# Performance work log

Hardware: AMD Instinct MI355X
Metric: run time of the kernel (lower is better)

The kernel has to match this reference:

```python
import jax, jax.numpy as jnp
import numpy as np

B, S, IN_DIM, H, NH, DH, OUT_DIM, K, N_KB, L, DFF = 32, 128, 1024, 1024, 8, 128, 256, 10, 500000, 2, 2048


def setup_inputs() -> dict:
    key = jax.random.key(0)
    ks = jax.random.split(key, 16)
    def rn(k, shape, scale=0.02):
        return jax.random.normal(k, shape, jnp.float32) * scale
    return {
        "x": jax.random.normal(ks[0], (B, S, IN_DIM), jnp.float32),
        "ctx": jax.random.normal(ks[1], (B, 1, IN_DIM), jnp.float32),
        "indices": jax.random.randint(ks[2], (B, S, K), 0, N_KB),
        "KB_embs": jax.random.normal(ks[3], (N_KB, OUT_DIM), jnp.float32),
        "W_in": rn(ks[4], (IN_DIM, H)), "b_in": jnp.zeros((H,), jnp.float32),
        "Wqkv": rn(ks[5], (L, H, 3 * H)), "bqkv": jnp.zeros((L, 3 * H), jnp.float32),
        "Wo": rn(ks[6], (L, H, H)), "bo": jnp.zeros((L, H), jnp.float32),
        "ln1_g": jnp.ones((L, H), jnp.float32), "ln1_b": jnp.zeros((L, H), jnp.float32),
        "W1": rn(ks[7], (L, H, DFF)), "b1": jnp.zeros((L, DFF), jnp.float32),
        "W2": rn(ks[8], (L, DFF, H)), "b2": jnp.zeros((L, H), jnp.float32),
        "ln2_g": jnp.ones((L, H), jnp.float32), "ln2_b": jnp.zeros((L, H), jnp.float32),
        "W_out": rn(ks[9], (H, OUT_DIM)), "b_out": jnp.zeros((OUT_DIM,), jnp.float32),
        "ds_W1": rn(ks[10], (OUT_DIM, OUT_DIM)), "ds_b1": jnp.zeros((OUT_DIM,), jnp.float32),
        "ds_W2": rn(ks[11], (OUT_DIM, 1)), "ds_b2": jnp.zeros((1,), jnp.float32),
        "cs_W1": rn(ks[12], (OUT_DIM, OUT_DIM)), "cs_b1": jnp.zeros((OUT_DIM,), jnp.float32),
        "cs_W2": rn(ks[13], (OUT_DIM, 1)), "cs_b2": jnp.zeros((1,), jnp.float32),
    }


def _ln(x, g, b, eps=1e-5):
    m = x.mean(-1, keepdims=True)
    v = ((x - m) ** 2).mean(-1, keepdims=True)
    return (x - m) * jax.lax.rsqrt(v + eps) * g + b


def _encoder_layer(h, Wqkv, bqkv, Wo, bo, g1, bn1, W1, b1, W2, b2, g2, bn2):
    # h: (Sq, Bt, H). PyTorch default batch_first=False -> axis 0 is the attended
    # sequence axis (here the data batch axis B, exactly as the original code runs).
    Sq, Bt, Hd = h.shape
    q, k, v = jnp.split(h @ Wqkv + bqkv, 3, axis=-1)
    q = q.reshape(Sq, Bt, NH, DH)
    k = k.reshape(Sq, Bt, NH, DH)
    v = v.reshape(Sq, Bt, NH, DH)
    att = jnp.einsum('sbhd,tbhd->bhst', q, k) * (1.0 / (DH ** 0.5))
    att = jax.nn.softmax(att, axis=-1)
    o = jnp.einsum('bhst,tbhd->sbhd', att, v).reshape(Sq, Bt, Hd)
    h = _ln(h + o @ Wo + bo, g1, bn1)          # post-norm, eps=1e-5
    ff = jax.nn.relu(h @ W1 + b1) @ W2 + b2    # default dim_feedforward=2048, relu
    return _ln(h + ff, g2, bn2)


def _forward(x, ctx, indices, KB_embs, W_in, b_in, Wqkv, bqkv, Wo, bo, ln1_g, ln1_b,
             W1, b1, W2, b2, ln2_g, ln2_b, W_out, b_out,
             ds_W1, ds_b1, ds_W2, ds_b2, cs_W1, cs_b1, cs_W2, cs_b2):
    h = jnp.concatenate([ctx, x], axis=1)          # (B, S+1, in_dim)
    h = jax.nn.relu(h @ W_in + b_in)               # mapper head (dropout off in eval)
    for l in range(Wqkv.shape[0]):
        h = _encoder_layer(h, Wqkv[l], bqkv[l], Wo[l], bo[l], ln1_g[l], ln1_b[l],
                           W1[l], b1[l], W2[l], b2[l], ln2_g[l], ln2_b[l])
    out = h @ W_out + b_out                        # (B, S+1, out_dim)
    ctx_e, pred = out[:, :1], out[:, 1:]
    idx = jnp.where(indices < 0, 0, indices)       # indices[indices == -1] = 0
    cand = KB_embs[idx]                            # (B, S, K, out_dim) gather
    d = cand - pred[:, :, None, :]
    c = ctx_e[:, :, None, :] * cand
    ds = jax.nn.relu(d @ ds_W1 + ds_b1) @ ds_W2 + ds_b2   # distance_score (B,S,K,1)
    cs = jax.nn.relu(c @ cs_W1 + cs_b1) @ cs_W2 + cs_b2   # context_score: computed but unused by original output
    del cs
    cand_out = jnp.concatenate([ds, cand], axis=-1)       # (B, S, K, 1+out_dim)
    return pred, cand_out


def reference(x, ctx, indices, KB_embs, W_in, b_in, Wqkv, bqkv, Wo, bo, ln1_g, ln1_b,
              W1, b1, W2, b2, ln2_g, ln2_b, W_out, b_out,
              ds_W1, ds_b1, ds_W2, ds_b2, cs_W1, cs_b1, cs_W2, cs_b2):
    return _forward(x, ctx, indices, KB_embs, W_in, b_in, Wqkv, bqkv, Wo, bo,
                    ln1_g, ln1_b, W1, b1, W2, b2, ln2_g, ln2_b, W_out, b_out,
                    ds_W1, ds_b1, ds_W2, ds_b2, cs_W1, cs_b1, cs_W2, cs_b2)
```

## Files before the change

### kernel.cpp

```cpp
#include <hip/hip_runtime.h>
#include <hip/hip_bf16.h>

typedef __attribute__((ext_vector_type(4))) float f32x4;
typedef __attribute__((ext_vector_type(8))) short s16x8;
typedef __attribute__((ext_vector_type(4))) unsigned short u16x4;
typedef __attribute__((ext_vector_type(8))) __bf16 bf16x8;

#define B_      32
#define S_      128
#define SEQ     129
#define IN_DIM  1024
#define HD      1024
#define NHEAD   8
#define DH      128
#define OUT_DIM 256
#define KC      10
#define DFF     2048
#define MROWS   (B_*SEQ)
#define MPAD    4224
#define NCAND   (B_*S_*KC)

__device__ __forceinline__ short f2bf(float f) {
  unsigned u = __builtin_bit_cast(unsigned, f);
  u += 0x7FFFu + ((u >> 16) & 1u);
  return (short)(u >> 16);
}
__device__ __forceinline__ float bf2f(short s) {
  return __builtin_bit_cast(float, ((unsigned)(unsigned short)s) << 16);
}
__device__ __forceinline__ void gload16(const short* g, short* l) {
  __builtin_amdgcn_global_load_lds(
      (const __attribute__((address_space(1))) unsigned*)g,
      (__attribute__((address_space(3))) unsigned*)l, 16, 0, 0);
}
__device__ __forceinline__ f32x4 mfma16(s16x8 a, s16x8 b, f32x4 c) {
  return __builtin_amdgcn_mfma_f32_16x16x32_bf16(
      __builtin_bit_cast(bf16x8, a), __builtin_bit_cast(bf16x8, b), c, 0, 0, 0);
}

__global__ __launch_bounds__(256) void prologue(
    const float* __restrict__ W_in,  const float* __restrict__ Wqkv,
    const float* __restrict__ Wo,    const float* __restrict__ W1,
    const float* __restrict__ W2,    const float* __restrict__ W_out,
    const float* __restrict__ dsW1,
    short* __restrict__ WinT,  short* __restrict__ WqkvT,
    short* __restrict__ WoT,   short* __restrict__ W1T,
    short* __restrict__ W2T,   short* __restrict__ WoutT,
    short* __restrict__ dsW1T,
    const float* __restrict__ x, const float* __restrict__ ctx,
    short* __restrict__ hin) {
  const int b = blockIdx.x;
  if (b >= 17728) {
    const int r = b - 17728;
    const int bb = r / SEQ, t = r % SEQ;
    const float* src = (t == 0) ? (ctx + (size_t)bb * IN_DIM)
                                : (x + ((size_t)bb * S_ + (t - 1)) * IN_DIM);
    f32x4 v = *(const f32x4*)(src + threadIdx.x * 4);
    u16x4 o;
    o.x = (unsigned short)f2bf(v.x); o.y = (unsigned short)f2bf(v.y);
    o.z = (unsigned short)f2bf(v.z); o.w = (unsigned short)f2bf(v.w);
    *(u16x4*)(hin + (size_t)r * IN_DIM + threadIdx.x * 4) = o;
    return;
  }
  const float* src; short* dst; int K, N, local;
  if (b < 1024)       { src = W_in;  dst = WinT;  K = 1024; N = 1024; local = b; }
  else if (b < 7168)  { int l = (b - 1024) / 3072; local = (b - 1024) % 3072;
                        src = Wqkv + (size_t)l * 1024 * 3072;
                        dst = WqkvT + (size_t)l * 3072 * 1024; K = 1024; N = 3072; }
  else if (b < 9216)  { int l = (b - 7168) / 1024; local = (b - 7168) % 1024;
                        src = Wo + (size_t)l * 1024 * 1024;
                        dst = WoT + (size_t)l * 1024 * 1024; K = 1024; N = 1024; }
  else if (b < 13312) { int l = (b - 9216) / 2048; local = (b - 9216) % 2048;
                        src = W1 + (size_t)l * 1024 * 2048;
                        dst = W1T + (size_t)l * 2048 * 1024; K = 1024; N = 2048; }
  else if (b < 17408) { int l = (b - 13312) / 2048; local = (b - 13312) % 2048;
                        src = W2 + (size_t)l * 2048 * 1024;
                        dst = W2T + (size_t)l * 1024 * 2048; K = 2048; N = 1024; }
  else if (b < 17664) { local = b - 17408; src = W_out; dst = WoutT; K = 1024; N = 256; }
  else                { local = b - 17664; src = dsW1;  dst = dsW1T; K = 256;  N = 256; }
  const int tilesX = N >> 5;
  const int n0 = (local % tilesX) << 5, k0 = (local / tilesX) << 5;

  __shared__ float tile[32][33];
  const int tx = threadIdx.x & 31, ty = threadIdx.x >> 5;
#pragma unroll
  for (int i = 0; i < 4; ++i)
    tile[ty + i * 8][tx] = src[(size_t)(k0 + ty + i * 8) * N + n0 + tx];
  __syncthreads();
#pragma unroll
  for (int i = 0; i < 4; ++i)
    dst[(size_t)(n0 + ty + i * 8) * K + k0 + tx] = f2bf(tile[tx][ty + i * 8]);
}

template <int EPI, bool SPLIT, typename OutT>
__global__ __launch_bounds__(256) void gemm_bt(const short* __restrict__ A,
                                               const short* __restrict__ Bt,
                                               const float* __restrict__ bias,
                                               OutT* __restrict__ C,
                                               short* __restrict__ Pb,
                                               int M, int N, int K,
                                               int gm, int gn, int groupM,
                                               int kper) {
  __shared__ alignas(16) short As0[4096], As1[4096];
  __shared__ alignas(16) short Bs0[4096], Bs1[4096];
  const int tid = threadIdx.x;
  const int lane = tid & 63, wave = tid >> 6;
  const int wr = wave >> 1, wc = wave & 1;

  const int nwg = gm * gn;
  int orig = blockIdx.x;
  int split = 0;
  if constexpr (SPLIT) { split = orig / nwg; orig %= nwg; }
  const int xcd = orig & 7, kk = orig >> 3;
  const int q = nwg >> 3, r = nwg & 7;
  const int wg = (xcd < r ? xcd * (q + 1) : r * (q + 1) + (xcd - r) * q) + kk;
  const int tpg = groupM * gn;
  const int grp = wg / tpg, rem = wg % tpg;
  const int g0 = grp * groupM;
  const int gsz = (groupM < gm - g0) ? groupM : (gm - g0);
  const int bm = (g0 + rem % gsz) * 128;
  const int bn = (rem / gsz) * 128;
  const int kbase = SPLIT ? split * kper : 0;

  const short* pa[2];
  const short* pb[2];
#pragma unroll
  for (int i = 0; i < 2; ++i) {
    const int idx = i * 256 + tid;
    const int rr = idx >> 2, ss = idx & 3, gg = ss ^ ((rr >> 1) & 3);
    pa[i] = A + (size_t)(bm + rr) * K + kbase + gg * 8;
    pb[i] = Bt + (size_t)(bn + rr) * K + kbase + gg * 8;
  }

  auto stage = [&](short* aBuf, short* bBuf, int t) {
    const int kofs = t << 5;
    gload16(pa[0] + kofs, aBuf + wave * 512);
    gload16(pa[1] + kofs, aBuf + 2048 + wave * 512);
    gload16(pb[0] + kofs, bBuf + wave * 512);
    gload16(pb[1] + kofs, bBuf + 2048 + wave * 512);
  };

  const int lrow = lane & 15, ks = lane >> 4;
  const int sx = (lrow >> 1) & 3;
  const int koff = ((ks ^ sx) << 3);

  f32x4 acc[4][4] = {};

  auto compute = [&](const short* as, const short* bs) {
    s16x8 af[4], bfr[4];
#pragma unroll
    for (int m = 0; m < 4; ++m)
      af[m] = *(const s16x8*)&as[(wr * 64 + m * 16 + lrow) * 32 + koff];
#pragma unroll
    for (int n = 0; n < 4; ++n)
      bfr[n] = *(const s16x8*)&bs[(wc * 64 + n * 16 + lrow) * 32 + koff];
#pragma unroll
    for (int m = 0; m < 4; ++m)
#pragma unroll
      for (int n = 0; n < 4; ++n)
        asm("v_mfma_f32_16x16x32_bf16 %0, %1, %2, %0"
            : "+v"(acc[m][n]) : "v"(af[m]), "v"(bfr[n]));
  };

  const int NT = (SPLIT ? kper : K) >> 5;
  stage(As0, Bs0, 0);
  __syncthreads();
  for (int t = 0; t < NT; t += 2) {
    stage(As1, Bs1, t + 1);
    compute(As0, Bs0);
    __syncthreads();
    if (t + 2 < NT) stage(As0, Bs0, t + 2);
    compute(As1, Bs1);
    __syncthreads();
  }

  const int lg4 = ks << 2;
#pragma unroll
  for (int n = 0; n < 4; ++n) {
    const int col = bn + wc * 64 + n * 16 + lrow;
    const float bvx = SPLIT ? 0.f : bias[col];
#pragma unroll
    for (int m = 0; m < 4; ++m) {
#pragma unroll
      for (int r2 = 0; r2 < 4; ++r2) {
        const int row = bm + wr * 64 + m * 16 + lg4 + r2;
        if constexpr (SPLIT) {
          Pb[((size_t)split * MPAD + row) * N + col] = f2bf(acc[m][n][r2]);
        } else {
          if (row < M) {
            float v = acc[m][n][r2] + bvx;
            if (EPI == 1) v = fmaxf(v, 0.f);
            if constexpr (__is_same(OutT, float)) {
              C[(size_t)row * N + col] = v;
            } else {
              C[(size_t)row * N + col] = f2bf(v);
            }
          }
        }
      }
    }
  }
}

template <int EPI>
__global__ __launch_bounds__(256) void reduce_cast(const short* __restrict__ P,
                                                   const float* __restrict__ bias,
                                                   short* __restrict__ out,
                                                   int N, int nsplit) {
  const int row = blockIdx.x;
  for (int c = threadIdx.x * 4; c < N; c += 1024) {
    f32x4 s = *(const f32x4*)(bias + c);
    for (int sp = 0; sp < nsplit; ++sp) {
      u16x4 pv = *(const u16x4*)(P + ((size_t)sp * MPAD + row) * N + c);
      s.x += bf2f((short)pv.x); s.y += bf2f((short)pv.y);
      s.z += bf2f((short)pv.z); s.w += bf2f((short)pv.w);
    }
    if (EPI == 1) {
      s.x = fmaxf(s.x, 0.f); s.y = fmaxf(s.y, 0.f);
      s.z = fmaxf(s.z, 0.f); s.w = fmaxf(s.w, 0.f);
    }
    u16x4 y;
    y.x = (unsigned short)f2bf(s.x); y.y = (unsigned short)f2bf(s.y);
    y.z = (unsigned short)f2bf(s.z); y.w = (unsigned short)f2bf(s.w);
    *(u16x4*)(out + (size_t)row * N + c) = y;
  }
}

__global__ __launch_bounds__(256) void reduce_ln(const short* __restrict__ P,
                                                 const float* __restrict__ bias,
                                                 const float* __restrict__ g,
                                                 const float* __restrict__ bb,
                                                 short* __restrict__ h) {
  const int r = blockIdx.x, tid = threadIdx.x;
  f32x4 s = *(const f32x4*)(bias + tid * 4);
  {
    u16x4 p0 = *(const u16x4*)(P + (size_t)r * 1024 + tid * 4);
    u16x4 p1 = *(const u16x4*)(P + ((size_t)MPAD + r) * 1024 + tid * 4);
    s.x += bf2f((short)p0.x) + bf2f((short)p1.x);
    s.y += bf2f((short)p0.y) + bf2f((short)p1.y);
    s.z += bf2f((short)p0.z) + bf2f((short)p1.z);
    s.w += bf2f((short)p0.w) + bf2f((short)p1.w);
  }
  const u16x4 hv = *(const u16x4*)(h + (size_t)r * 1024 + tid * 4);
  float s0 = s.x + bf2f((short)hv.x);
  float s1 = s.y + bf2f((short)hv.y);
  float s2 = s.z + bf2f((short)hv.z);
  float s3 = s.w + bf2f((short)hv.w);
  float ls = s0 + s1 + s2 + s3;
  float l2 = s0 * s0 + s1 * s1 + s2 * s2 + s3 * s3;
#pragma unroll
  for (int off = 32; off > 0; off >>= 1) {
    ls += __shfl_down(ls, off);
    l2 += __shfl_down(l2, off);
  }
  __shared__ float red[8];
  const int wave = tid >> 6, lane = tid & 63;
  if (lane == 0) { red[wave * 2] = ls; red[wave * 2 + 1] = l2; }
  __syncthreads();
  if (tid == 0) {
    float a = 0.f, b2 = 0.f;
    for (int w = 0; w < 4; ++w) { a += red[w * 2]; b2 += red[w * 2 + 1]; }
    red[0] = a; red[1] = b2;
  }
  __syncthreads();
  const float mean = red[0] * (1.f / HD);
  const float var  = red[1] * (1.f / HD) - mean * mean;
  const float inv  = rsqrtf(var + 1e-5f);
  const f32x4 gv = *(const f32x4*)(g + tid * 4);
  const f32x4 bv = *(const f32x4*)(bb + tid * 4);
  u16x4 y;
  y.x = (unsigned short)f2bf((s0 - mean) * inv * gv.x + bv.x);
  y.y = (unsigned short)f2bf((s1 - mean) * inv * gv.y + bv.y);
  y.z = (unsigned short)f2bf((s2 - mean) * inv * gv.z + bv.z);
  y.w = (unsigned short)f2bf((s3 - mean) * inv * gv.w + bv.w);
  *(u16x4*)(h + (size_t)r * 1024 + tid * 4) = y;
}

__global__ __launch_bounds__(64) void reduce_wout(const short* __restrict__ P,
                                                  const float* __restrict__ bias,
                                                  float* __restrict__ pred) {
  const int r = blockIdx.x;
  const int b = r / SEQ, t = r % SEQ;
  if (t == 0) return;
  const int c = threadIdx.x * 4;
  f32x4 s = *(const f32x4*)(bias + c);
#pragma unroll
  for (int sp = 0; sp < 4; ++sp) {
    u16x4 pv = *(const u16x4*)(P + ((size_t)sp * MPAD + r) * 256 + c);
    s.x += bf2f((short)pv.x); s.y += bf2f((short)pv.y);
    s.z += bf2f((short)pv.z); s.w += bf2f((short)pv.w);
  }
  *(f32x4*)(pred + ((size_t)b * S_ + (t - 1)) * 256 + c) = s;
}

__global__ __launch_bounds__(256) void attention_mfma(const short* __restrict__ qkv,
                                                      short* __restrict__ o) {
  __shared__ alignas(16) short qs[4][32][136];
  __shared__ alignas(16) short ksb[4][32][136];
  __shared__ alignas(16) short vsb[4][32][136];
  __shared__ float psb[4][32][33];
  const int tid = threadIdx.x, lane = tid & 63, w = tid >> 6;
  const int gw = blockIdx.x * 4 + w;
  const int t = gw >> 3, hd = gw & 7;
  short (*q)[136] = qs[w];
  short (*k)[136] = ksb[w];
  short (*v)[136] = vsb[w];
  float (*ps)[33] = psb[w];

#pragma unroll
  for (int c = lane; c < 512; c += 64) {
    const int bb = c >> 4, d8 = (c & 15) << 3;
    const size_t base = ((size_t)(bb * SEQ + t)) * (3 * HD) + hd * DH + d8;
    *(s16x8*)&q[bb][d8] = *(const s16x8*)(qkv + base);
    *(s16x8*)&k[bb][d8] = *(const s16x8*)(qkv + base + HD);
    *(s16x8*)&v[bb][d8] = *(const s16x8*)(qkv + base + 2 * HD);
  }

  const int lrow = lane & 15, ksl = lane >> 4;
  const float scale = 0.08838834764831845f;

  f32x4 pacc[2][2] = {};
#pragma unroll
  for (int kst = 0; kst < 4; ++kst) {
    s16x8 aq[2], bk[2];
#pragma unroll
    for (int m = 0; m < 2; ++m)
      aq[m] = *(const s16x8*)&q[m * 16 + lrow][kst * 32 + ksl * 8];
#pragma unroll
    for (int n = 0; n < 2; ++n)
      bk[n] = *(const s16x8*)&k[n * 16 + lrow][kst * 32 + ksl * 8];
#pragma unroll
    for (int m = 0; m < 2; ++m)
#pragma unroll
      for (int n = 0; n < 2; ++n)
        pacc[m][n] = mfma16(aq[m], bk[n], pacc[m][n]);
  }
#pragma unroll
  for (int m = 0; m < 2; ++m)
#pragma unroll
    for (int n = 0; n < 2; ++n)
#pragma unroll
      for (int r = 0; r < 4; ++r)
        ps[m * 16 + ksl * 4 + r][n * 16 + lrow] = pacc[m][n][r] * scale;

  if (lane < 32) {
    float mx = -1e30f;
#pragma unroll
    for (int j = 0; j < 32; ++j) mx = fmaxf(mx, ps[lane][j]);
    float sum = 0.f;
    float e[32];
#pragma unroll
    for (int j = 0; j < 32; ++j) { e[j] = __expf(ps[lane][j] - mx); sum += e[j]; }
    const float inv = 1.f / sum;
#pragma unroll
    for (int j = 0; j < 32; ++j) ps[lane][j] = e[j] * inv;
  }

  s16x8 pa[2];
#pragma unroll
  for (int m = 0; m < 2; ++m) {
    const float* pr = &ps[m * 16 + lrow][ksl * 8];
#pragma unroll
    for (int j = 0; j < 8; ++j) pa[m][j] = f2bf(pr[j]);
  }
  f32x4 oacc[2][8] = {};
#pragma unroll
  for (int n = 0; n < 8; ++n) {
    s16x8 bv;
#pragma unroll
    for (int r = 0; r < 8; ++r)
      bv[r] = v[ksl * 8 + r][n * 16 + lrow];
#pragma unroll
    for (int m = 0; m < 2; ++m)
      oacc[m][n] = mfma16(pa[m], bv, oacc[m][n]);
  }
#pragma unroll
  for (int m = 0; m < 2; ++m)
#pragma unroll
    for (int n = 0; n < 8; ++n)
#pragma unroll
      for (int r = 0; r < 4; ++r) {
        const int i = m * 16 + ksl * 4 + r;
        const int d = n * 16 + lrow;
        o[((size_t)(i * SEQ + t)) * HD + hd * DH + d] = f2bf(oacc[m][n][r]);
      }
}

__global__ __launch_bounds__(256) void cand_score(
    const float* __restrict__ pred, const int* __restrict__ indices,
    const float* __restrict__ KB, const short* __restrict__ W1T,
    const float* __restrict__ b1v, const float* __restrict__ w2v,
    const float* __restrict__ b2v, float* __restrict__ cand_out) {
  __shared__ alignas(16) short Asw[8 * 2048];
  __shared__ alignas(16) short Bs0[8192], Bs1[8192];
  __shared__ float red[64];
  const int tid = threadIdx.x;
  const int lane = tid & 63, wave = tid >> 6;
  const int lrow = lane & 15, ks = lane >> 4;
  const int sx = (lrow >> 1) & 3;
  const int koff = ((ks ^ sx) << 3);
  const int r0 = blockIdx.x << 6;

  {
    const int l4 = lane << 2;
    const int kslice = l4 >> 5, kslot = (l4 >> 3) & 3, kin = l4 & 7;
#pragma unroll
    for (int it = 0; it < 16; ++it) {
      const int rr = wave + (it << 2);
      const int R = r0 + rr;
      const int bs = R / KC, k = R - bs * KC;
      int idx = indices[(size_t)bs * KC + k];
      if (idx < 0) idx = 0;
      f32x4 cv = *(const f32x4*)(KB + (size_t)idx * OUT_DIM + l4);
      f32x4 pv = *(const f32x4*)(pred + (size_t)bs * OUT_DIM + l4);
      float* co = cand_out + (size_t)R * 257 + 1 + l4;
      co[0] = cv.x; co[1] = cv.y; co[2] = cv.z; co[3] = cv.w;
      u16x4 dv;
      dv.x = (unsigned short)f2bf(cv.x - pv.x);
      dv.y = (unsigned short)f2bf(cv.y - pv.y);
      dv.z = (unsigned short)f2bf(cv.z - pv.z);
      dv.w = (unsigned short)f2bf(cv.w - pv.w);
      const int rsw = (rr >> 1) & 3;
      *(u16x4*)&Asw[kslice * 2048 + rr * 32 + ((kslot ^ rsw) << 3) + kin] = dv;
    }
  }
  if (tid < 64) red[tid] = 0.f;

  const short* pb[4];
#pragma unroll
  for (int i = 0; i < 4; ++i) {
    const int idx2 = i * 256 + tid;
    const int rr = idx2 >> 2, ss = idx2 & 3, gg = ss ^ ((rr >> 1) & 3);
    pb[i] = W1T + (size_t)rr * 256 + gg * 8;
  }
  auto stageB = [&](short* buf, int t) {
#pragma unroll
    for (int i = 0; i < 4; ++i)
      gload16(pb[i] + (t << 5), buf + i * 2048 + wave * 512);
  };

  f32x4 acc[4][4] = {};
  auto computeDS = [&](const short* as, const short* bsrc) {
    s16x8 af[4], bfr[4];
#pragma unroll
    for (int m = 0; m < 4; ++m)
      af[m] = *(const s16x8*)&as[(m * 16 + lrow) * 32 + koff];
#pragma unroll
    for (int n = 0; n < 4; ++n)
      bfr[n] = *(const s16x8*)&bsrc[(wave * 64 + n * 16 + lrow) * 32 + koff];
#pragma unroll
    for (int m = 0; m < 4; ++m)
#pragma unroll
      for (int n = 0; n < 4; ++n)
        asm("v_mfma_f32_16x16x32_bf16 %0, %1, %2, %0"
            : "+v"(acc[m][n]) : "v"(af[m]), "v"(bfr[n]));
  };

  stageB(Bs0, 0);
  __syncthreads();
  for (int t = 0; t < 8; t += 2) {
    stageB(Bs1, t + 1);
    computeDS(Asw + t * 2048, Bs0);
    __syncthreads();
    if (t + 2 < 8) stageB(Bs0, t + 2);
    computeDS(Asw + (t + 1) * 2048, Bs1);
    __syncthreads();
  }

  float w2r[4], b1r[4];
#pragma unroll
  for (int n = 0; n < 4; ++n) {
    const int col = wave * 64 + n * 16 + lrow;
    w2r[n] = w2v[col];
    b1r[n] = b1v[col];
  }
#pragma unroll
  for (int m = 0; m < 4; ++m) {
#pragma unroll
    for (int r2 = 0; r2 < 4; ++r2) {
      float part = 0.f;
#pragma unroll
      for (int n = 0; n < 4; ++n)
        part += fmaxf(acc[m][n][r2] + b1r[n], 0.f) * w2r[n];
      part += __shfl_xor(part, 1);
      part += __shfl_xor(part, 2);
      part += __shfl_xor(part, 4);
      part += __shfl_xor(part, 8);
      if (lrow == 0) atomicAdd(&red[m * 16 + ks * 4 + r2], part);
    }
  }
  __syncthreads();
  if (tid < 64)
    cand_out[(size_t)(r0 + tid) * 257] = red[tid] + b2v[0];
}

extern "C" void kernel_launch(void* const* d_in, const int* in_sizes, int n_in,
                              void* d_out, int out_size, void* d_ws, size_t ws_size,
                              hipStream_t stream) {
  const float* x      = (const float*)d_in[0];
  const float* ctx    = (const float*)d_in[1];
  const int*   indices= (const int*)d_in[2];
  const float* KB     = (const float*)d_in[3];
  const float* W_in   = (const float*)d_in[4];
  const float* b_in   = (const float*)d_in[5];
  const float* Wqkv   = (const float*)d_in[6];
  const float* bqkv   = (const float*)d_in[7];
  const float* Wo     = (const float*)d_in[8];
  const float* bo     = (const float*)d_in[9];
  const float* ln1_g  = (const float*)d_in[10];
  const float* ln1_b  = (const float*)d_in[11];
  const float* W1     = (const float*)d_in[12];
  const float* b1     = (const float*)d_in[13];
  const float* W2     = (const float*)d_in[14];
  const float* b2     = (const float*)d_in[15];
  const float* ln2_g  = (const float*)d_in[16];
  const float* ln2_b  = (const float*)d_in[17];
  const float* W_out  = (const float*)d_in[18];
  const float* b_out  = (const float*)d_in[19];
  const float* ds_W1  = (const float*)d_in[20];
  const float* ds_b1  = (const float*)d_in[21];
  const float* ds_W2  = (const float*)d_in[22];
  const float* ds_b2  = (const float*)d_in[23];

  char* p = (char*)d_ws;
  auto alloc = [&](size_t bytes) {
    char* q = p;
    p += (bytes + 255) & ~(size_t)255;
    return q;
  };
  short* h    = (short*)alloc((size_t)MPAD * HD * 2);
  short* tmp1 = (short*)alloc((size_t)MPAD * 3 * HD * 2);
  short* tmp2 = (short*)alloc((size_t)MPAD * HD * 2);
  short* part = (short*)alloc((size_t)2 * MPAD * HD * 2);
  short* WinT  = (short*)alloc((size_t)HD * IN_DIM * 2);
  short* WqkvT = (short*)alloc((size_t)2 * 3 * HD * HD * 2);
  short* WoT   = (short*)alloc((size_t)2 * HD * HD * 2);
  short* W1T   = (short*)alloc((size_t)2 * DFF * HD * 2);
  short* W2T   = (short*)alloc((size_t)2 * HD * DFF * 2);
  short* WoutT = (short*)alloc((size_t)OUT_DIM * HD * 2);
  short* dsW1T = (short*)alloc((size_t)OUT_DIM * OUT_DIM * 2);

  prologue<<<17728 + MROWS, 256, 0, stream>>>(
      W_in, Wqkv, Wo, W1, W2, W_out, ds_W1,
      WinT, WqkvT, WoT, W1T, W2T, WoutT, dsW1T, x, ctx, tmp2);

  gemm_bt<0, true, short><<<33 * 8 * 2, 256, 0, stream>>>(
      tmp2, WinT, nullptr, nullptr, part, MROWS, 1024, 1024, 33, 8, 8, 512);
  reduce_cast<1><<<MROWS, 256, 0, stream>>>(part, b_in, h, 1024, 2);

  for (int l = 0; l < 2; ++l) {
    gemm_bt<0, false, short><<<33 * 24, 256, 0, stream>>>(
        h, WqkvT + (size_t)l * 3072 * 1024, bqkv + l * 3072, tmp1, nullptr,
        MROWS, 3072, 1024, 33, 24, 8, 0);
    attention_mfma<<<258, 256, 0, stream>>>(tmp1, tmp2);
    gemm_bt<0, true, short><<<33 * 8 * 2, 256, 0, stream>>>(
        tmp2, WoT + (size_t)l * 1024 * 1024, nullptr, nullptr, part,
        MROWS, 1024, 1024, 33, 8, 8, 512);
    reduce_ln<<<MROWS, 256, 0, stream>>>(part, bo + l * 1024,
                                         ln1_g + l * 1024, ln1_b + l * 1024, h);
    gemm_bt<1, false, short><<<33 * 16, 256, 0, stream>>>(
        h, W1T + (size_t)l * 2048 * 1024, b1 + l * 2048, tmp1, nullptr,
        MROWS, 2048, 1024, 33, 16, 8, 0);
    gemm_bt<0, true, short><<<33 * 8 * 2, 256, 0, stream>>>(
        tmp1, W2T + (size_t)l * 1024 * 2048, nullptr, nullptr, part,
        MROWS, 1024, 2048, 33, 8, 4, 1024);
    reduce_ln<<<MROWS, 256, 0, stream>>>(part, b2 + l * 1024,
                                         ln2_g + l * 1024, ln2_b + l * 1024, h);
  }

  float* pred = (float*)d_out;
  float* cand_out = (float*)d_out + (size_t)B_ * S_ * OUT_DIM;

  gemm_bt<0, true, float><<<33 * 2 * 4, 256, 0, stream>>>(
      h, WoutT, nullptr, nullptr, part, MROWS, 256, 1024, 33, 2, 8, 256);
  reduce_wout<<<MROWS, 64, 0, stream>>>(part, b_out, pred);

  cand_score<<<NCAND / 64, 256, 0, stream>>>(pred, indices, KB, dsW1T,
                                             ds_b1, ds_W2, ds_b2, cand_out);
}
```

Measured before the change: 409.4 us.

## Double split-K factor for output GEMMs and load attention Q/K directly from global

The split-K count for the W_in, Wo, W2 and W_out GEMMs doubles, giving twice as many workgroups on the 256-CU device, and the partial buffer grows to match. The reduce_ln kernel is templated on the split count, and reduce_wout now sums eight partials. Attention stops staging Q and K in LDS and loads MFMA operands straight from global memory, cutting LDS use and a staging pass. The cost is more partial-sum traffic to write and re-read, and uncoalesced global loads for Q and K.

```diff
diff --git a/kernel.cpp b/kernel.cpp
--- a/kernel.cpp
+++ b/kernel.cpp
@@ -226,6 +226,7 @@
   }
 }
 
+template <int NSPLIT>
 __global__ __launch_bounds__(256) void reduce_ln(const short* __restrict__ P,
                                                  const float* __restrict__ bias,
                                                  const float* __restrict__ g,
@@ -233,13 +234,11 @@
                                                  short* __restrict__ h) {
   const int r = blockIdx.x, tid = threadIdx.x;
   f32x4 s = *(const f32x4*)(bias + tid * 4);
-  {
-    u16x4 p0 = *(const u16x4*)(P + (size_t)r * 1024 + tid * 4);
-    u16x4 p1 = *(const u16x4*)(P + ((size_t)MPAD + r) * 1024 + tid * 4);
-    s.x += bf2f((short)p0.x) + bf2f((short)p1.x);
-    s.y += bf2f((short)p0.y) + bf2f((short)p1.y);
-    s.z += bf2f((short)p0.z) + bf2f((short)p1.z);
-    s.w += bf2f((short)p0.w) + bf2f((short)p1.w);
+#pragma unroll
+  for (int sp = 0; sp < NSPLIT; ++sp) {
+    u16x4 pv = *(const u16x4*)(P + ((size_t)sp * MPAD + r) * 1024 + tid * 4);
+    s.x += bf2f((short)pv.x); s.y += bf2f((short)pv.y);
+    s.z += bf2f((short)pv.z); s.w += bf2f((short)pv.w);
   }
   const u16x4 hv = *(const u16x4*)(h + (size_t)r * 1024 + tid * 4);
   float s0 = s.x + bf2f((short)hv.x);
@@ -285,7 +284,7 @@
   const int c = threadIdx.x * 4;
   f32x4 s = *(const f32x4*)(bias + c);
 #pragma unroll
-  for (int sp = 0; sp < 4; ++sp) {
+  for (int sp = 0; sp < 8; ++sp) {
     u16x4 pv = *(const u16x4*)(P + ((size_t)sp * MPAD + r) * 256 + c);
     s.x += bf2f((short)pv.x); s.y += bf2f((short)pv.y);
     s.z += bf2f((short)pv.z); s.w += bf2f((short)pv.w);
@@ -295,28 +294,22 @@
 
 __global__ __launch_bounds__(256) void attention_mfma(const short* __restrict__ qkv,
                                                       short* __restrict__ o) {
-  __shared__ alignas(16) short qs[4][32][136];
-  __shared__ alignas(16) short ksb[4][32][136];
   __shared__ alignas(16) short vsb[4][32][136];
   __shared__ float psb[4][32][33];
   const int tid = threadIdx.x, lane = tid & 63, w = tid >> 6;
   const int gw = blockIdx.x * 4 + w;
   const int t = gw >> 3, hd = gw & 7;
-  short (*q)[136] = qs[w];
-  short (*k)[136] = ksb[w];
   short (*v)[136] = vsb[w];
   float (*ps)[33] = psb[w];
+  const int lrow = lane & 15, ksl = lane >> 4;
 
 #pragma unroll
   for (int c = lane; c < 512; c += 64) {
     const int bb = c >> 4, d8 = (c & 15) << 3;
     const size_t base = ((size_t)(bb * SEQ + t)) * (3 * HD) + hd * DH + d8;
-    *(s16x8*)&q[bb][d8] = *(const s16x8*)(qkv + base);
-    *(s16x8*)&k[bb][d8] = *(const s16x8*)(qkv + base + HD);
     *(s16x8*)&v[bb][d8] = *(const s16x8*)(qkv + base + 2 * HD);
   }
 
-  const int lrow = lane & 15, ksl = lane >> 4;
   const float scale = 0.08838834764831845f;
 
   f32x4 pacc[2][2] = {};
@@ -324,11 +317,12 @@
   for (int kst = 0; kst < 4; ++kst) {
     s16x8 aq[2], bk[2];
 #pragma unroll
-    for (int m = 0; m < 2; ++m)
-      aq[m] = *(const s16x8*)&q[m * 16 + lrow][kst * 32 + ksl * 8];
-#pragma unroll
-    for (int n = 0; n < 2; ++n)
-      bk[n] = *(const s16x8*)&k[n * 16 + lrow][kst * 32 + ksl * 8];
+    for (int m = 0; m < 2; ++m) {
+      const size_t base = ((size_t)((m * 16 + lrow) * SEQ + t)) * (3 * HD)
+                        + hd * DH + kst * 32 + ksl * 8;
+      aq[m] = *(const s16x8*)(qkv + base);
+      bk[m] = *(const s16x8*)(qkv + base + HD);
+    }
 #pragma unroll
     for (int m = 0; m < 2; ++m)
 #pragma unroll
@@ -531,7 +525,7 @@
   short* h    = (short*)alloc((size_t)MPAD * HD * 2);
   short* tmp1 = (short*)alloc((size_t)MPAD * 3 * HD * 2);
   short* tmp2 = (short*)alloc((size_t)MPAD * HD * 2);
-  short* part = (short*)alloc((size_t)2 * MPAD * HD * 2);
+  short* part = (short*)alloc((size_t)4 * MPAD * HD * 2);
   short* WinT  = (short*)alloc((size_t)HD * IN_DIM * 2);
   short* WqkvT = (short*)alloc((size_t)2 * 3 * HD * HD * 2);
   short* WoT   = (short*)alloc((size_t)2 * HD * HD * 2);
@@ -544,35 +538,35 @@
       W_in, Wqkv, Wo, W1, W2, W_out, ds_W1,
       WinT, WqkvT, WoT, W1T, W2T, WoutT, dsW1T, x, ctx, tmp2);
 
-  gemm_bt<0, true, short><<<33 * 8 * 2, 256, 0, stream>>>(
-      tmp2, WinT, nullptr, nullptr, part, MROWS, 1024, 1024, 33, 8, 8, 512);
-  reduce_cast<1><<<MROWS, 256, 0, stream>>>(part, b_in, h, 1024, 2);
+  gemm_bt<0, true, short><<<33 * 8 * 4, 256, 0, stream>>>(
+      tmp2, WinT, nullptr, nullptr, part, MROWS, 1024, 1024, 33, 8, 8, 256);
+  reduce_cast<1><<<MROWS, 256, 0, stream>>>(part, b_in, h, 1024, 4);
 
   for (int l = 0; l < 2; ++l) {
     gemm_bt<0, false, short><<<33 * 24, 256, 0, stream>>>(
         h, WqkvT + (size_t)l * 3072 * 1024, bqkv + l * 3072, tmp1, nullptr,
         MROWS, 3072, 1024, 33, 24, 8, 0);
     attention_mfma<<<258, 256, 0, stream>>>(tmp1, tmp2);
-    gemm_bt<0, true, short><<<33 * 8 * 2, 256, 0, stream>>>(
+    gemm_bt<0, true, short><<<33 * 8 * 4, 256, 0, stream>>>(
         tmp2, WoT + (size_t)l * 1024 * 1024, nullptr, nullptr, part,
-        MROWS, 1024, 1024, 33, 8, 8, 512);
-    reduce_ln<<<MROWS, 256, 0, stream>>>(part, bo + l * 1024,
-                                         ln1_g + l * 1024, ln1_b + l * 1024, h);
+        MROWS, 1024, 1024, 33, 8, 8, 256);
+    reduce_ln<4><<<MROWS, 256, 0, stream>>>(part, bo + l * 1024,
+                                            ln1_g + l * 1024, ln1_b + l * 1024, h);
     gemm_bt<1, false, short><<<33 * 16, 256, 0, stream>>>(
         h, W1T + (size_t)l * 2048 * 1024, b1 + l * 2048, tmp1, nullptr,
         MROWS, 2048, 1024, 33, 16, 8, 0);
-    gemm_bt<0, true, short><<<33 * 8 * 2, 256, 0, stream>>>(
+    gemm_bt<0, true, short><<<33 * 8 * 4, 256, 0, stream>>>(
         tmp1, W2T + (size_t)l * 1024 * 2048, nullptr, nullptr, part,
-        MROWS, 1024, 2048, 33, 8, 4, 1024);
-    reduce_ln<<<MROWS, 256, 0, stream>>>(part, b2 + l * 1024,
-                                         ln2_g + l * 1024, ln2_b + l * 1024, h);
+        MROWS, 1024, 2048, 33, 8, 4, 512);
+    reduce_ln<4><<<MROWS, 256, 0, stream>>>(part, b2 + l * 1024,
+                                            ln2_g + l * 1024, ln2_b + l * 1024, h);
   }
 
   float* pred = (float*)d_out;
   float* cand_out = (float*)d_out + (size_t)B_ * S_ * OUT_DIM;
 
-  gemm_bt<0, true, float><<<33 * 2 * 4, 256, 0, stream>>>(
-      h, WoutT, nullptr, nullptr, part, MROWS, 256, 1024, 33, 2, 8, 256);
+  gemm_bt<0, true, float><<<33 * 2 * 8, 256, 0, stream>>>(
+      h, WoutT, nullptr, nullptr, part, MROWS, 256, 1024, 33, 2, 8, 128);
   reduce_wout<<<MROWS, 64, 0, stream>>>(part, b_out, pred);
 
   cand_score<<<NCAND / 64, 256, 0, stream>>>(pred, indices, KB, dsW1T,
```

Result: slower. 425.8 us (+4.0%).
